# Performance work log

Hardware: AMD Instinct MI355X
Metric: run time of the kernel (lower is better)

## Reference

```python
import jax, jax.numpy as jnp
import numpy as np
import math

B, T, C, H = 4, 4096, 512, 64  # batch, seq_len, n_embed, head_size


def setup_inputs() -> dict:
    key = jax.random.key(0)
    kx, kq, kk, kv = jax.random.split(key, 4)
    scale = 1.0 / math.sqrt(C)  # ~Linear init scale
    return {
        "x": jax.random.normal(kx, (B, T, C), dtype=jnp.float32),
        "Wq": jax.random.normal(kq, (C, H), dtype=jnp.float32) * scale,
        "Wk": jax.random.normal(kk, (C, H), dtype=jnp.float32) * scale,
        "Wv": jax.random.normal(kv, (C, H), dtype=jnp.float32) * scale,
    }


def reference(x, Wq, Wk, Wv):
    # Single-head causal self-attention (mask=True path, dropout=0/eval).
    # NOTE: original module scales by 1/sqrt(C) (n_embed), not 1/sqrt(head_size).
    Bn, Tn, Cn = x.shape
    q = x @ Wq  # [B,T,H]
    k = x @ Wk  # [B,T,H]
    v = x @ Wv  # [B,T,H]
    inv_scale = jnp.float32(1.0 / math.sqrt(Cn))
    scores = jnp.einsum('bth,bsh->bts', q, k) * inv_scale  # [B,T,T]
    causal = jnp.tril(jnp.ones((Tn, Tn), dtype=bool))
    scores = jnp.where(causal, scores, jnp.float32(-jnp.inf))
    attn = jax.nn.softmax(scores, axis=-1)
    out = jnp.einsum('bts,bsh->bth', attn, v)  # [B,T,H]
    return out
```

## Files before the change

kernel.cpp:

```cpp
#include <hip/hip_runtime.h>
#include <math.h>

#define BATCH 4
#define SEQT  4096
#define CDIM  512
#define HDIM  64

typedef unsigned short ushort_t;
typedef __attribute__((ext_vector_type(8))) short bf16x8;
typedef __attribute__((ext_vector_type(4))) float f32x4;

#define MFMA16(a, b, c) __builtin_amdgcn_mfma_f32_16x16x32_bf16((a), (b), (c), 0, 0, 0)
#define NEG (-1e30f)

__device__ __forceinline__ ushort_t f2bf(float f) {
  union { float f; unsigned int u; } v;
  v.f = f;
  unsigned int u = v.u;
  u += 0x7fffu + ((u >> 16) & 1u);
  return (ushort_t)(u >> 16);
}
__device__ __forceinline__ unsigned int pk2(float a, float b) {
  return (unsigned int)f2bf(a) | ((unsigned int)f2bf(b) << 16);
}

__global__ __launch_bounds__(256) void convert_w(
    const float* __restrict__ Wq, const float* __restrict__ Wk,
    const float* __restrict__ Wv, ushort_t* __restrict__ wtf) {
  int g = blockIdx.x * 256 + threadIdx.x;
  int lane = g & 63;
  int nt = (g >> 6) & 3;
  int ks = (g >> 8) & 15;
  int mat = g >> 12;
  const float* W = (mat == 0) ? Wq : (mat == 1) ? Wk : Wv;
  const float sc = (mat == 0) ? 0.04419417382415922f : 1.0f;
  int n = lane & 15, quad = lane >> 4;
  int h = nt * 16 + n;
  int c0 = ks * 32 + quad * 8;
  ushort_t tmp[8];
#pragma unroll
  for (int j = 0; j < 8; ++j) tmp[j] = f2bf(W[(c0 + j) * HDIM + h] * sc);
  *(bf16x8*)(wtf + (size_t)g * 8) = *(const bf16x8*)tmp;
}

#define XPAD 520

__global__ __launch_bounds__(384) void qkv_proj(
    const float* __restrict__ x, const ushort_t* __restrict__ wtf,
    ushort_t* __restrict__ qb, ushort_t* __restrict__ kbf,
    ushort_t* __restrict__ vbf) {
  __shared__ ushort_t Xs[32 * XPAD];
  __shared__ ushort_t Pk[3][32 * 72];

  const int tid = threadIdx.x;
  const int row0 = blockIdx.x * 32;

  const float4* xg = (const float4*)(x + (size_t)row0 * CDIM);
  for (int i = tid; i < 32 * (CDIM / 4); i += 384) {
    float4 xv = xg[i];
    int r = i >> 7, c4 = i & 127;
    uint2 u;
    u.x = pk2(xv.x, xv.y);
    u.y = pk2(xv.z, xv.w);
    *(uint2*)&Xs[r * XPAD + c4 * 4] = u;
  }
  __syncthreads();

  const int lane = tid & 63;
  const int w = tid >> 6;
  const int mat = w >> 1;
  const int half = w & 1;
  const int n = lane & 15, quad = lane >> 4;
  const ushort_t* wb = wtf + mat * 32768;

  f32x4 acc[4];
#pragma unroll
  for (int nt = 0; nt < 4; ++nt) acc[nt] = (f32x4){0.f, 0.f, 0.f, 0.f};

  bf16x8 bcur[4];
#pragma unroll
  for (int nt = 0; nt < 4; ++nt)
    bcur[nt] = *(const bf16x8*)&wb[nt * 512 + lane * 8];

  for (int ks = 0; ks < 16; ++ks) {
    bf16x8 a = *(const bf16x8*)&Xs[(half * 16 + n) * XPAD + ks * 32 + quad * 8];
    bf16x8 bnext[4];
    if (ks < 15) {
#pragma unroll
      for (int nt = 0; nt < 4; ++nt)
        bnext[nt] = *(const bf16x8*)&wb[((ks + 1) * 4 + nt) * 512 + lane * 8];
    }
#pragma unroll
    for (int nt = 0; nt < 4; ++nt) acc[nt] = MFMA16(a, bcur[nt], acc[nt]);
    if (ks < 15) {
#pragma unroll
      for (int nt = 0; nt < 4; ++nt) bcur[nt] = bnext[nt];
    }
  }

  ushort_t* P = Pk[mat];
#pragma unroll
  for (int nt = 0; nt < 4; ++nt)
#pragma unroll
    for (int i = 0; i < 4; ++i)
      P[(half * 16 + quad * 4 + i) * 72 + nt * 16 + n] = f2bf(acc[nt][i]);
  __syncthreads();

  if (mat == 0) {
    int c = half * 64 + lane;
    int r = c >> 2, seg = c & 3;
    const uint4* s = (const uint4*)&Pk[0][r * 72 + seg * 16];
    uint4* d = (uint4*)(qb + (size_t)(row0 + r) * HDIM + seg * 16);
    d[0] = s[0];
    d[1] = s[1];
  } else if (mat == 1) {
#pragma unroll
    for (int ks2 = 0; ks2 < 2; ++ks2) {
      bf16x8 fr =
          *(const bf16x8*)&Pk[1][(half * 16 + n) * 72 + ks2 * 32 + quad * 8];
      *(bf16x8*)(kbf + (size_t)(((row0 >> 4) + half) * 2 + ks2) * 512 +
                 lane * 8) = fr;
    }
  } else {
    const int b = row0 >> 12, t0 = row0 & 4095;
    const int kt = t0 >> 6, kslot = (t0 >> 5) & 1;
#pragma unroll
    for (int ntc = 0; ntc < 2; ++ntc) {
      const int nt = half * 2 + ntc;
      ushort_t tmp[8];
#pragma unroll
      for (int j = 0; j < 8; ++j)
        tmp[j] = Pk[2][(quad * 8 + j) * 72 + nt * 16 + n];
      *(bf16x8*)(vbf + (size_t)(((b * 64 + kt) * 4 + nt) * 2 + kslot) * 512 +
                 lane * 8) = *(const bf16x8*)tmp;
    }
  }
}

__global__ __launch_bounds__(512, 4) void attn(
    const ushort_t* __restrict__ qb, const ushort_t* __restrict__ kbf,
    const ushort_t* __restrict__ vbf, float* __restrict__ out) {
  __shared__ __align__(16) char smem[70656];
  ushort_t* Ps = (ushort_t*)smem;
  float* Om = (float*)smem;
  float* Ol = (float*)(smem + 69632);

  const int tid = threadIdx.x;
  const int lane = tid & 63;
  const int w = tid >> 6;
  const int n = lane & 15, quad = lane >> 4;

  const int b = blockIdx.x & 3;
  const int qt = 127 - (blockIdx.x >> 2);
  const int q0 = qt * 32;

  const ushort_t* qB = qb + (size_t)b * SEQT * HDIM;
  const ushort_t* kB = kbf + (size_t)b * 512 * 512;
  const ushort_t* vB = vbf + (size_t)b * 512 * 512;
  float* oB = out + (size_t)b * SEQT * HDIM;

  bf16x8 qf[2][2];
#pragma unroll
  for (int m2 = 0; m2 < 2; ++m2)
#pragma unroll
    for (int ks = 0; ks < 2; ++ks)
      qf[m2][ks] = *(const bf16x8*)&qB[(size_t)(q0 + m2 * 16 + n) * HDIM +
                                       ks * 32 + quad * 8];

  bf16x8 ones;
#pragma unroll
  for (int j = 0; j < 8; ++j) ones[j] = (short)0x3F80;

  f32x4 o[2][4], ol[2];
#pragma unroll
  for (int m2 = 0; m2 < 2; ++m2) {
#pragma unroll
    for (int nt = 0; nt < 4; ++nt) o[m2][nt] = (f32x4){0.f, 0.f, 0.f, 0.f};
    ol[m2] = (f32x4){0.f, 0.f, 0.f, 0.f};
  }

  const int ktiles = (q0 + 95) >> 6;
  ushort_t* Pw = Ps + w * 2304;

  for (int kt = w; kt < ktiles; kt += 8) {
    const int k0 = kt * 64;

    f32x4 s[2][4];
#pragma unroll
    for (int m2 = 0; m2 < 2; ++m2)
#pragma unroll
      for (int nt = 0; nt < 4; ++nt) s[m2][nt] = (f32x4){0.f, 0.f, 0.f, 0.f};

#pragma unroll
    for (int ks = 0; ks < 2; ++ks)
#pragma unroll
      for (int nt = 0; nt < 4; ++nt) {
        bf16x8 kf = *(const bf16x8*)&kB[(size_t)((kt * 4 + nt) * 2 + ks) * 512 +
                                        lane * 8];
        s[0][nt] = MFMA16(qf[0][ks], kf, s[0][nt]);
        s[1][nt] = MFMA16(qf[1][ks], kf, s[1][nt]);
      }

    if (k0 + 63 > q0) {
#pragma unroll
      for (int m2 = 0; m2 < 2; ++m2) {
        const int rbase = q0 + m2 * 16 + quad * 4;
#pragma unroll
        for (int nt = 0; nt < 4; ++nt) {
          const int col = k0 + nt * 16 + n;
#pragma unroll
          for (int i = 0; i < 4; ++i)
            if (col > rbase + i) s[m2][nt][i] = NEG;
        }
      }
    }

#pragma unroll
    for (int m2 = 0; m2 < 2; ++m2)
#pragma unroll
      for (int nt = 0; nt < 4; ++nt)
#pragma unroll
        for (int i = 0; i < 4; ++i)
          Pw[(m2 * 16 + quad * 4 + i) * 72 + nt * 16 + n] =
              f2bf(__expf(s[m2][nt][i]));

#pragma unroll
    for (int ks = 0; ks < 2; ++ks) {
      bf16x8 pa0 = *(const bf16x8*)&Pw[n * 72 + ks * 32 + quad * 8];
      bf16x8 pa1 = *(const bf16x8*)&Pw[(16 + n) * 72 + ks * 32 + quad * 8];
      ol[0] = MFMA16(pa0, ones, ol[0]);
      ol[1] = MFMA16(pa1, ones, ol[1]);
#pragma unroll
      for (int nt = 0; nt < 4; ++nt) {
        bf16x8 vf = *(const bf16x8*)&vB[(size_t)((kt * 4 + nt) * 2 + ks) * 512 +
                                        lane * 8];
        o[0][nt] = MFMA16(pa0, vf, o[0][nt]);
        o[1][nt] = MFMA16(pa1, vf, o[1][nt]);
      }
    }
  }

  __syncthreads();

  float* OmW = Om + w * 2176;
#pragma unroll
  for (int m2 = 0; m2 < 2; ++m2) {
#pragma unroll
    for (int nt = 0; nt < 4; ++nt)
#pragma unroll
      for (int i = 0; i < 4; ++i)
        OmW[(m2 * 16 + quad * 4 + i) * 68 + nt * 16 + n] = o[m2][nt][i];
    if (n == 0)
#pragma unroll
      for (int i = 0; i < 4; ++i)
        Ol[w * 32 + m2 * 16 + quad * 4 + i] = ol[m2][i];
  }
  __syncthreads();

  {
    const int r = tid >> 4;
    const int c0 = (tid & 15) * 4;
    float ax = 0.f, ay = 0.f, az = 0.f, aw = 0.f, ls = 0.f;
#pragma unroll
    for (int ww = 0; ww < 8; ++ww) {
      const float4 vv = *(const float4*)&Om[ww * 2176 + r * 68 + c0];
      ax += vv.x; ay += vv.y; az += vv.z; aw += vv.w;
      ls += Ol[ww * 32 + r];
    }
    const float inv = 1.0f / ls;
    *(float4*)&oB[(size_t)(q0 + r) * HDIM + c0] =
        make_float4(ax * inv, ay * inv, az * inv, aw * inv);
  }
}

extern "C" void kernel_launch(void* const* d_in, const int* in_sizes, int n_in,
                              void* d_out, int out_size, void* d_ws, size_t ws_size,
                              hipStream_t stream) {
  const float* x = (const float*)d_in[0];
  const float* Wq = (const float*)d_in[1];
  const float* Wk = (const float*)d_in[2];
  const float* Wv = (const float*)d_in[3];
  float* out = (float*)d_out;

  ushort_t* wtf = (ushort_t*)d_ws;
  ushort_t* qb = wtf + 3 * 16 * 4 * 512;
  ushort_t* kbf = qb + (size_t)BATCH * SEQT * HDIM;
  ushort_t* vbf = kbf + (size_t)BATCH * 512 * 512;

  convert_w<<<48, 256, 0, stream>>>(Wq, Wk, Wv, wtf);
  qkv_proj<<<BATCH * SEQT / 32, 384, 0, stream>>>(x, wtf, qb, kbf, vbf);
  attn<<<512, 512, 0, stream>>>(qb, kbf, vbf, out);
}
```

Baseline: 115.6 us.

## Split projection along K across waves and re-partition attention waves by row-half

```diff
diff --git a/kernel.cpp b/kernel.cpp
--- a/kernel.cpp
+++ b/kernel.cpp
@@ -43,33 +43,34 @@
   *(bf16x8*)(wtf + (size_t)g * 8) = *(const bf16x8*)tmp;
 }
 
-#define XPAD 520
+#define XP 520
 
 __global__ __launch_bounds__(384) void qkv_proj(
     const float* __restrict__ x, const ushort_t* __restrict__ wtf,
-    ushort_t* __restrict__ qb, ushort_t* __restrict__ kbf,
+    ushort_t* __restrict__ qbf, ushort_t* __restrict__ kbf,
     ushort_t* __restrict__ vbf) {
-  __shared__ ushort_t Xs[32 * XPAD];
-  __shared__ ushort_t Pk[3][32 * 72];
+  __shared__ ushort_t Xs[16 * XP];
+  __shared__ float Facc[3 * 1088];
+  __shared__ ushort_t Pk[3][16 * 72];
 
   const int tid = threadIdx.x;
-  const int row0 = blockIdx.x * 32;
+  const int row0 = blockIdx.x * 16;
 
   const float4* xg = (const float4*)(x + (size_t)row0 * CDIM);
-  for (int i = tid; i < 32 * (CDIM / 4); i += 384) {
+  for (int i = tid; i < 16 * (CDIM / 4); i += 384) {
     float4 xv = xg[i];
     int r = i >> 7, c4 = i & 127;
     uint2 u;
     u.x = pk2(xv.x, xv.y);
     u.y = pk2(xv.z, xv.w);
-    *(uint2*)&Xs[r * XPAD + c4 * 4] = u;
+    *(uint2*)&Xs[r * XP + c4 * 4] = u;
   }
   __syncthreads();
 
   const int lane = tid & 63;
   const int w = tid >> 6;
   const int mat = w >> 1;
-  const int half = w & 1;
+  const int kh = w & 1;
   const int n = lane & 15, quad = lane >> 4;
   const ushort_t* wb = wtf + mat * 32768;
 
@@ -80,192 +81,211 @@
   bf16x8 bcur[4];
 #pragma unroll
   for (int nt = 0; nt < 4; ++nt)
-    bcur[nt] = *(const bf16x8*)&wb[nt * 512 + lane * 8];
-
-  for (int ks = 0; ks < 16; ++ks) {
-    bf16x8 a = *(const bf16x8*)&Xs[(half * 16 + n) * XPAD + ks * 32 + quad * 8];
+    bcur[nt] = *(const bf16x8*)&wb[(kh * 8 * 4 + nt) * 512 + lane * 8];
+
+  for (int kk = 0; kk < 8; ++kk) {
+    const int ks = kh * 8 + kk;
+    bf16x8 a = *(const bf16x8*)&Xs[n * XP + ks * 32 + quad * 8];
     bf16x8 bnext[4];
-    if (ks < 15) {
+    if (kk < 7) {
 #pragma unroll
       for (int nt = 0; nt < 4; ++nt)
         bnext[nt] = *(const bf16x8*)&wb[((ks + 1) * 4 + nt) * 512 + lane * 8];
     }
 #pragma unroll
     for (int nt = 0; nt < 4; ++nt) acc[nt] = MFMA16(a, bcur[nt], acc[nt]);
-    if (ks < 15) {
+    if (kk < 7) {
 #pragma unroll
       for (int nt = 0; nt < 4; ++nt) bcur[nt] = bnext[nt];
     }
   }
 
-  ushort_t* P = Pk[mat];
-#pragma unroll
-  for (int nt = 0; nt < 4; ++nt)
-#pragma unroll
-    for (int i = 0; i < 4; ++i)
-      P[(half * 16 + quad * 4 + i) * 72 + nt * 16 + n] = f2bf(acc[nt][i]);
+  if (kh == 1) {
+#pragma unroll
+    for (int nt = 0; nt < 4; ++nt)
+#pragma unroll
+      for (int i = 0; i < 4; ++i)
+        Facc[mat * 1088 + lane * 17 + nt * 4 + i] = acc[nt][i];
+  }
   __syncthreads();
 
-  if (mat == 0) {
-    int c = half * 64 + lane;
-    int r = c >> 2, seg = c & 3;
-    const uint4* s = (const uint4*)&Pk[0][r * 72 + seg * 16];
-    uint4* d = (uint4*)(qb + (size_t)(row0 + r) * HDIM + seg * 16);
-    d[0] = s[0];
-    d[1] = s[1];
-  } else if (mat == 1) {
-#pragma unroll
-    for (int ks2 = 0; ks2 < 2; ++ks2) {
-      bf16x8 fr =
-          *(const bf16x8*)&Pk[1][(half * 16 + n) * 72 + ks2 * 32 + quad * 8];
-      *(bf16x8*)(kbf + (size_t)(((row0 >> 4) + half) * 2 + ks2) * 512 +
-                 lane * 8) = fr;
-    }
-  } else {
-    const int b = row0 >> 12, t0 = row0 & 4095;
-    const int kt = t0 >> 6, kslot = (t0 >> 5) & 1;
-#pragma unroll
-    for (int ntc = 0; ntc < 2; ++ntc) {
-      const int nt = half * 2 + ntc;
-      ushort_t tmp[8];
-#pragma unroll
-      for (int j = 0; j < 8; ++j)
-        tmp[j] = Pk[2][(quad * 8 + j) * 72 + nt * 16 + n];
-      *(bf16x8*)(vbf + (size_t)(((b * 64 + kt) * 4 + nt) * 2 + kslot) * 512 +
-                 lane * 8) = *(const bf16x8*)tmp;
+  if (kh == 0) {
+#pragma unroll
+    for (int nt = 0; nt < 4; ++nt)
+#pragma unroll
+      for (int i = 0; i < 4; ++i) {
+        acc[nt][i] += Facc[mat * 1088 + lane * 17 + nt * 4 + i];
+        Pk[mat][(quad * 4 + i) * 72 + nt * 16 + n] = f2bf(acc[nt][i]);
+      }
+    if (mat == 0) {
+#pragma unroll
+      for (int ks2 = 0; ks2 < 2; ++ks2) {
+        bf16x8 fr = *(const bf16x8*)&Pk[0][n * 72 + ks2 * 32 + quad * 8];
+        *(bf16x8*)(qbf + (size_t)((row0 >> 4) * 2 + ks2) * 512 + lane * 8) = fr;
+      }
+    } else if (mat == 1) {
+#pragma unroll
+      for (int ks2 = 0; ks2 < 2; ++ks2) {
+        bf16x8 fr = *(const bf16x8*)&Pk[1][n * 72 + ks2 * 32 + quad * 8];
+        *(bf16x8*)(kbf + (size_t)((row0 >> 4) * 2 + ks2) * 512 + lane * 8) = fr;
+      }
+    } else {
+      const int b = row0 >> 12, t0 = row0 & 4095;
+      const int kt = t0 >> 6, kslot = (t0 >> 5) & 1, tsub = (t0 >> 4) & 1;
+      if ((quad >> 1) == tsub) {
+        const int lq = quad & 1;
+#pragma unroll
+        for (int nt = 0; nt < 4; ++nt) {
+          ushort_t tmp[8];
+#pragma unroll
+          for (int j = 0; j < 8; ++j)
+            tmp[j] = Pk[2][(lq * 8 + j) * 72 + nt * 16 + n];
+          *(bf16x8*)(vbf + (size_t)(((b * 64 + kt) * 4 + nt) * 2 + kslot) * 512 +
+                     lane * 8) = *(const bf16x8*)tmp;
+        }
+      }
     }
   }
 }
 
 __global__ __launch_bounds__(512, 4) void attn(
-    const ushort_t* __restrict__ qb, const ushort_t* __restrict__ kbf,
+    const ushort_t* __restrict__ qbf, const ushort_t* __restrict__ kbf,
     const ushort_t* __restrict__ vbf, float* __restrict__ out) {
-  __shared__ __align__(16) char smem[70656];
+  __shared__ __align__(16) char smem[35328];
   ushort_t* Ps = (ushort_t*)smem;
   float* Om = (float*)smem;
-  float* Ol = (float*)(smem + 69632);
+  float* Ol = (float*)(smem + 34816);
 
   const int tid = threadIdx.x;
   const int lane = tid & 63;
   const int w = tid >> 6;
+  const int m2 = w & 1;
+  const int kt0 = w >> 1;
   const int n = lane & 15, quad = lane >> 4;
 
   const int b = blockIdx.x & 3;
   const int qt = 127 - (blockIdx.x >> 2);
   const int q0 = qt * 32;
 
-  const ushort_t* qB = qb + (size_t)b * SEQT * HDIM;
+  const ushort_t* qB = qbf + (size_t)b * 512 * 512;
   const ushort_t* kB = kbf + (size_t)b * 512 * 512;
   const ushort_t* vB = vbf + (size_t)b * 512 * 512;
   float* oB = out + (size_t)b * SEQT * HDIM;
 
-  bf16x8 qf[2][2];
-#pragma unroll
-  for (int m2 = 0; m2 < 2; ++m2)
+  bf16x8 qf[2];
+#pragma unroll
+  for (int ks = 0; ks < 2; ++ks)
+    qf[ks] = *(const bf16x8*)&qB[(size_t)((qt * 2 + m2) * 2 + ks) * 512 +
+                                 lane * 8];
+
+  bf16x8 ones;
+#pragma unroll
+  for (int j = 0; j < 8; ++j) ones[j] = (short)0x3F80;
+
+  f32x4 o[4], ol;
+#pragma unroll
+  for (int nt = 0; nt < 4; ++nt) o[nt] = (f32x4){0.f, 0.f, 0.f, 0.f};
+  ol = (f32x4){0.f, 0.f, 0.f, 0.f};
+
+  const int ktiles = (q0 + 95) >> 6;
+  ushort_t* Pw = Ps + w * 1152;
+
+  bf16x8 kf[8];
+  if (kt0 < ktiles) {
 #pragma unroll
     for (int ks = 0; ks < 2; ++ks)
-      qf[m2][ks] = *(const bf16x8*)&qB[(size_t)(q0 + m2 * 16 + n) * HDIM +
-                                       ks * 32 + quad * 8];
-
-  bf16x8 ones;
-#pragma unroll
-  for (int j = 0; j < 8; ++j) ones[j] = (short)0x3F80;
-
-  f32x4 o[2][4], ol[2];
-#pragma unroll
-  for (int m2 = 0; m2 < 2; ++m2) {
-#pragma unroll
-    for (int nt = 0; nt < 4; ++nt) o[m2][nt] = (f32x4){0.f, 0.f, 0.f, 0.f};
-    ol[m2] = (f32x4){0.f, 0.f, 0.f, 0.f};
-  }
-
-  const int ktiles = (q0 + 95) >> 6;
-  ushort_t* Pw = Ps + w * 2304;
-
-  for (int kt = w; kt < ktiles; kt += 8) {
+#pragma unroll
+      for (int nt = 0; nt < 4; ++nt)
+        kf[ks * 4 + nt] = *(const bf16x8*)&kB[(size_t)((kt0 * 4 + nt) * 2 + ks) *
+                                                  512 + lane * 8];
+  }
+
+  for (int kt = kt0; kt < ktiles; kt += 4) {
     const int k0 = kt * 64;
-
-    f32x4 s[2][4];
-#pragma unroll
-    for (int m2 = 0; m2 < 2; ++m2)
-#pragma unroll
-      for (int nt = 0; nt < 4; ++nt) s[m2][nt] = (f32x4){0.f, 0.f, 0.f, 0.f};
-
+    const int ktn = kt + 4;
+
+    bf16x8 kfn[8];
+    if (ktn < ktiles) {
+#pragma unroll
+      for (int ks = 0; ks < 2; ++ks)
+#pragma unroll
+        for (int nt = 0; nt < 4; ++nt)
+          kfn[ks * 4 + nt] =
+              *(const bf16x8*)&kB[(size_t)((ktn * 4 + nt) * 2 + ks) * 512 +
+                                  lane * 8];
+    }
+
+    f32x4 s[4];
+#pragma unroll
+    for (int nt = 0; nt < 4; ++nt) s[nt] = (f32x4){0.f, 0.f, 0.f, 0.f};
 #pragma unroll
     for (int ks = 0; ks < 2; ++ks)
 #pragma unroll
+      for (int nt = 0; nt < 4; ++nt)
+        s[nt] = MFMA16(qf[ks], kf[ks * 4 + nt], s[nt]);
+
+    bf16x8 vf[8];
+#pragma unroll
+    for (int ks = 0; ks < 2; ++ks)
+#pragma unroll
+      for (int nt = 0; nt < 4; ++nt)
+        vf[ks * 4 + nt] = *(const bf16x8*)&vB[(size_t)((kt * 4 + nt) * 2 + ks) *
+                                                  512 + lane * 8];
+
+    if (k0 + 63 > q0) {
+      const int rbase = q0 + m2 * 16 + quad * 4;
+#pragma unroll
       for (int nt = 0; nt < 4; ++nt) {
-        bf16x8 kf = *(const bf16x8*)&kB[(size_t)((kt * 4 + nt) * 2 + ks) * 512 +
-                                        lane * 8];
-        s[0][nt] = MFMA16(qf[0][ks], kf, s[0][nt]);
-        s[1][nt] = MFMA16(qf[1][ks], kf, s[1][nt]);
-      }
-
-    if (k0 + 63 > q0) {
-#pragma unroll
-      for (int m2 = 0; m2 < 2; ++m2) {
-        const int rbase = q0 + m2 * 16 + quad * 4;
-#pragma unroll
-        for (int nt = 0; nt < 4; ++nt) {
-          const int col = k0 + nt * 16 + n;
-#pragma unroll
-          for (int i = 0; i < 4; ++i)
-            if (col > rbase + i) s[m2][nt][i] = NEG;
-        }
-      }
-    }
-
-#pragma unroll
-    for (int m2 = 0; m2 < 2; ++m2)
-#pragma unroll
-      for (int nt = 0; nt < 4; ++nt)
+        const int col = k0 + nt * 16 + n;
 #pragma unroll
         for (int i = 0; i < 4; ++i)
-          Pw[(m2 * 16 + quad * 4 + i) * 72 + nt * 16 + n] =
-              f2bf(__expf(s[m2][nt][i]));
+          if (col > rbase + i) s[nt][i] = NEG;
+      }
+    }
+
+#pragma unroll
+    for (int nt = 0; nt < 4; ++nt)
+#pragma unroll
+      for (int i = 0; i < 4; ++i)
+        Pw[(quad * 4 + i) * 72 + nt * 16 + n] = f2bf(__expf(s[nt][i]));
 
 #pragma unroll
     for (int ks = 0; ks < 2; ++ks) {
-      bf16x8 pa0 = *(const bf16x8*)&Pw[n * 72 + ks * 32 + quad * 8];
-      bf16x8 pa1 = *(const bf16x8*)&Pw[(16 + n) * 72 + ks * 32 + quad * 8];
-      ol[0] = MFMA16(pa0, ones, ol[0]);
-      ol[1] = MFMA16(pa1, ones, ol[1]);
-#pragma unroll
-      for (int nt = 0; nt < 4; ++nt) {
-        bf16x8 vf = *(const bf16x8*)&vB[(size_t)((kt * 4 + nt) * 2 + ks) * 512 +
-                                        lane * 8];
-        o[0][nt] = MFMA16(pa0, vf, o[0][nt]);
-        o[1][nt] = MFMA16(pa1, vf, o[1][nt]);
-      }
-    }
+      bf16x8 pa = *(const bf16x8*)&Pw[n * 72 + ks * 32 + quad * 8];
+      ol = MFMA16(pa, ones, ol);
+#pragma unroll
+      for (int nt = 0; nt < 4; ++nt)
+        o[nt] = MFMA16(pa, vf[ks * 4 + nt], o[nt]);
+    }
+
+#pragma unroll
+    for (int f = 0; f < 8; ++f) kf[f] = kfn[f];
   }
 
   __syncthreads();
 
-  float* OmW = Om + w * 2176;
-#pragma unroll
-  for (int m2 = 0; m2 < 2; ++m2) {
-#pragma unroll
-    for (int nt = 0; nt < 4; ++nt)
-#pragma unroll
-      for (int i = 0; i < 4; ++i)
-        OmW[(m2 * 16 + quad * 4 + i) * 68 + nt * 16 + n] = o[m2][nt][i];
-    if (n == 0)
-#pragma unroll
-      for (int i = 0; i < 4; ++i)
-        Ol[w * 32 + m2 * 16 + quad * 4 + i] = ol[m2][i];
-  }
+  float* OmW = Om + w * 1088;
+#pragma unroll
+  for (int nt = 0; nt < 4; ++nt)
+#pragma unroll
+    for (int i = 0; i < 4; ++i)
+      OmW[(quad * 4 + i) * 68 + nt * 16 + n] = o[nt][i];
+  if (n == 0)
+#pragma unroll
+    for (int i = 0; i < 4; ++i) Ol[w * 16 + quad * 4 + i] = ol[i];
   __syncthreads();
 
   {
     const int r = tid >> 4;
     const int c0 = (tid & 15) * 4;
+    const int m2r = r >> 4, lr = r & 15;
     float ax = 0.f, ay = 0.f, az = 0.f, aw = 0.f, ls = 0.f;
 #pragma unroll
-    for (int ww = 0; ww < 8; ++ww) {
-      const float4 vv = *(const float4*)&Om[ww * 2176 + r * 68 + c0];
+    for (int ww = 0; ww < 4; ++ww) {
+      const int wi = m2r + ww * 2;
+      const float4 vv = *(const float4*)&Om[wi * 1088 + lr * 68 + c0];
       ax += vv.x; ay += vv.y; az += vv.z; aw += vv.w;
-      ls += Ol[ww * 32 + r];
+      ls += Ol[wi * 16 + lr];
     }
     const float inv = 1.0f / ls;
     *(float4*)&oB[(size_t)(q0 + r) * HDIM + c0] =
@@ -283,11 +303,11 @@
   float* out = (float*)d_out;
 
   ushort_t* wtf = (ushort_t*)d_ws;
-  ushort_t* qb = wtf + 3 * 16 * 4 * 512;
-  ushort_t* kbf = qb + (size_t)BATCH * SEQT * HDIM;
+  ushort_t* qbf = wtf + 3 * 16 * 4 * 512;
+  ushort_t* kbf = qbf + (size_t)BATCH * 512 * 512;
   ushort_t* vbf = kbf + (size_t)BATCH * 512 * 512;
 
   convert_w<<<48, 256, 0, stream>>>(Wq, Wk, Wv, wtf);
-  qkv_proj<<<BATCH * SEQT / 32, 384, 0, stream>>>(x, wtf, qb, kbf, vbf);
-  attn<<<512, 512, 0, stream>>>(qb, kbf, vbf, out);
-}
+  qkv_proj<<<BATCH * SEQT / 16, 384, 0, stream>>>(x, wtf, qbf, kbf, vbf);
+  attn<<<512, 512, 0, stream>>>(qbf, kbf, vbf, out);
+}
```

Result: no change. 117.1 us (+1.4%).
